# Kernel tuning notes

Measured on AMD Instinct MI355X. Metric: run time of the kernel, lower is better.

Reference implementation:

```python
import jax, jax.numpy as jnp
import numpy as np

EPS = 1e-12  # matches torch F.normalize eps default scale behavior (1e-12)

def _l2_normalize(x):
    n = jnp.sqrt(jnp.sum(x * x, axis=-1, keepdims=True))
    return x / jnp.maximum(n, EPS)

def setup_inputs() -> dict:
    key = jax.random.key(0)
    k1, k2 = jax.random.split(key)
    B, K, D = 32768, 4096, 1024
    context_repr = jax.random.normal(k1, (B, D), dtype=jnp.float32)
    # matches nn.init.normal_(std=0.02)
    cluster_centers = 0.02 * jax.random.normal(k2, (K, D), dtype=jnp.float32)
    return {"context_repr": context_repr, "cluster_centers": cluster_centers}

def reference(context_repr, cluster_centers):
    # L2-normalize rows of both
    x = _l2_normalize(context_repr)        # [B, D]
    c = _l2_normalize(cluster_centers)     # [K, D]
    x2 = jnp.sum(x * x, axis=-1, keepdims=True)          # [B, 1]
    c2 = jnp.sum(c * c, axis=-1)[None, :]                # [1, K]
    d2 = x2 + c2 - 2.0 * jnp.einsum('bd,kd->bk', x, c)   # [B, K]
    hard = jnp.argmin(d2, axis=-1)                       # [B]
    # Gather the UN-normalized learnable centers (as in the torch code)
    cluster_embedding = cluster_centers[hard]            # [B, D]
    return cluster_embedding
```

## Files before the change

### kernel.cpp

```cpp
#include <hip/hip_runtime.h>
#include <stdint.h>

#define B_ROWS 32768
#define K_CENT 4096
#define D_DIM  1024
#define EPS_CAND 5e-4f

typedef unsigned short u16;
typedef __attribute__((ext_vector_type(8))) __bf16 bf16x8;
typedef __attribute__((ext_vector_type(4))) float f32x4;

__device__ inline u16 f32_to_bf16(float f) {
    unsigned u = __float_as_uint(f);
    u += 0x7FFFu + ((u >> 16) & 1u);
    return (u16)(u >> 16);
}
__device__ inline float bf16_to_f32(u16 h) {
    return __uint_as_float(((unsigned)h) << 16);
}
__device__ inline unsigned ord_of_f32(float f) {
    unsigned u = __float_as_uint(f);
    return (u & 0x80000000u) ? ~u : (u | 0x80000000u);
}
__device__ inline float f32_of_ord(unsigned o) {
    unsigned u = (o & 0x80000000u) ? (o & 0x7fffffffu) : ~o;
    return __uint_as_float(u);
}

__global__ __launch_bounds__(256) void prep_rows(
    const float* __restrict__ src, u16* __restrict__ hi, u16* __restrict__ lo,
    float* __restrict__ sq, float* __restrict__ den)
{
    __shared__ double sm[4];
    const int row = blockIdx.x, tid = threadIdx.x;
    const float4 v = reinterpret_cast<const float4*>(src + (size_t)row * D_DIM)[tid];
    double ss = (double)v.x * v.x + (double)v.y * v.y
              + (double)v.z * v.z + (double)v.w * v.w;
#pragma unroll
    for (int m = 1; m < 64; m <<= 1) ss += __shfl_xor(ss, m, 64);
    if ((tid & 63) == 0) sm[tid >> 6] = ss;
    __syncthreads();
    const double tot = sm[0] + sm[1] + sm[2] + sm[3];
    const float d = fmaxf(sqrtf((float)tot), 1e-12f);
    const float n0 = v.x / d, n1 = v.y / d, n2 = v.z / d, n3 = v.w / d;

    ushort4 h, l;
    h.x = f32_to_bf16(n0); l.x = f32_to_bf16(n0 - bf16_to_f32(h.x));
    h.y = f32_to_bf16(n1); l.y = f32_to_bf16(n1 - bf16_to_f32(h.y));
    h.z = f32_to_bf16(n2); l.z = f32_to_bf16(n2 - bf16_to_f32(h.z));
    h.w = f32_to_bf16(n3); l.w = f32_to_bf16(n3 - bf16_to_f32(h.w));
    reinterpret_cast<ushort4*>(hi + (size_t)row * D_DIM)[tid] = h;
    reinterpret_cast<ushort4*>(lo + (size_t)row * D_DIM)[tid] = l;

    double s2 = (double)n0 * n0 + (double)n1 * n1
              + (double)n2 * n2 + (double)n3 * n3;
#pragma unroll
    for (int m = 1; m < 64; m <<= 1) s2 += __shfl_xor(s2, m, 64);
    __syncthreads();
    if ((tid & 63) == 0) sm[tid >> 6] = s2;
    __syncthreads();
    if (tid == 0) {
        sq[row] = (float)(sm[0] + sm[1] + sm[2] + sm[3]);
        den[row] = d;
    }
}

#define BM 128
#define BN 128
#define BK 32

__device__ inline void gload_lds16(const u16* g, u16* l) {
    __builtin_amdgcn_global_load_lds(
        (const __attribute__((address_space(1))) void*)g,
        (__attribute__((address_space(3))) void*)l, 16, 0, 0);
}

__global__ __launch_bounds__(256, 2) void gemm_cand(
    const u16* __restrict__ Ahi, const u16* __restrict__ Alo,
    const u16* __restrict__ Bhi, const u16* __restrict__ Blo,
    const float* __restrict__ c2, unsigned long long* __restrict__ cand)
{
    __shared__ u16 sAhi[BM * BK], sAlo[BM * BK];
    __shared__ u16 sBhi[BN * BK], sBlo[BN * BK];

    const int tid = threadIdx.x, lane = tid & 63, w = tid >> 6;

    const int flat = blockIdx.x;
    const int swz = (flat & 7) * 1024 + (flat >> 3);
    const int bx = swz & 31;
    const int by = swz >> 5;
    const size_t arow0 = (size_t)by * BM;
    const size_t brow0 = (size_t)bx * BN;

    const int p0 = w * 128 + lane, p1 = p0 + 64;
    const int r0 = p0 >> 2, cc0 = (p0 & 3) ^ ((r0 >> 1) & 3);
    const int r1 = p1 >> 2, cc1 = (p1 & 3) ^ ((r1 >> 1) & 3);
    const size_t aoff0 = (arow0 + r0) * D_DIM + cc0 * 8;
    const size_t aoff1 = (arow0 + r1) * D_DIM + cc1 * 8;
    const size_t boff0 = (brow0 + r0) * D_DIM + cc0 * 8;
    const size_t boff1 = (brow0 + r1) * D_DIM + cc1 * 8;
    const int ldst0 = w * 1024, ldst1 = ldst0 + 512;

    const int fr = lane & 15, fc = lane >> 4;
    int aoff_lds[4], boff_lds[4];
#pragma unroll
    for (int i = 0; i < 4; ++i) {
        const int ar = (w >> 1) * 64 + i * 16 + fr;
        aoff_lds[i] = ar * BK + ((fc ^ ((ar >> 1) & 3)) * 8);
        const int br = (w & 1) * 64 + i * 16 + fr;
        boff_lds[i] = br * BK + ((fc ^ ((br >> 1) & 3)) * 8);
    }

    f32x4 acc[4][4] = {};

    for (int kt = 0; kt < D_DIM / BK; ++kt) {
        const int k0 = kt * BK;
        __syncthreads();
        gload_lds16(Ahi + aoff0 + k0, sAhi + ldst0);
        gload_lds16(Ahi + aoff1 + k0, sAhi + ldst1);
        gload_lds16(Alo + aoff0 + k0, sAlo + ldst0);
        gload_lds16(Alo + aoff1 + k0, sAlo + ldst1);
        gload_lds16(Bhi + boff0 + k0, sBhi + ldst0);
        gload_lds16(Bhi + boff1 + k0, sBhi + ldst1);
        gload_lds16(Blo + boff0 + k0, sBlo + ldst0);
        gload_lds16(Blo + boff1 + k0, sBlo + ldst1);
        __syncthreads();

        bf16x8 ah[4], al[4], bh[4], bl[4];
#pragma unroll
        for (int i = 0; i < 4; ++i) {
            ah[i] = *reinterpret_cast<const bf16x8*>(sAhi + aoff_lds[i]);
            al[i] = *reinterpret_cast<const bf16x8*>(sAlo + aoff_lds[i]);
            bh[i] = *reinterpret_cast<const bf16x8*>(sBhi + boff_lds[i]);
            bl[i] = *reinterpret_cast<const bf16x8*>(sBlo + boff_lds[i]);
        }
#pragma unroll
        for (int mi = 0; mi < 4; ++mi)
#pragma unroll
            for (int ni = 0; ni < 4; ++ni)
                acc[mi][ni] = __builtin_amdgcn_mfma_f32_16x16x32_bf16(ah[mi], bh[ni], acc[mi][ni], 0, 0, 0);
#pragma unroll
        for (int mi = 0; mi < 4; ++mi)
#pragma unroll
            for (int ni = 0; ni < 4; ++ni)
                acc[mi][ni] = __builtin_amdgcn_mfma_f32_16x16x32_bf16(ah[mi], bl[ni], acc[mi][ni], 0, 0, 0);
#pragma unroll
        for (int mi = 0; mi < 4; ++mi)
#pragma unroll
            for (int ni = 0; ni < 4; ++ni)
                acc[mi][ni] = __builtin_amdgcn_mfma_f32_16x16x32_bf16(al[mi], bh[ni], acc[mi][ni], 0, 0, 0);
    }

    const int group = bx * 2 + (w & 1);
    float c2v[4];
#pragma unroll
    for (int ni = 0; ni < 4; ++ni)
        c2v[ni] = c2[brow0 + (w & 1) * 64 + ni * 16 + fr];

#pragma unroll
    for (int mi = 0; mi < 4; ++mi) {
#pragma unroll
        for (int r = 0; r < 4; ++r) {
            unsigned long long bk = ~0ull;
#pragma unroll
            for (int ni = 0; ni < 4; ++ni) {
                const float d2a = c2v[ni] - 2.0f * acc[mi][ni][r];
                const unsigned col = (unsigned)(brow0 + (w & 1) * 64 + ni * 16 + fr);
                const unsigned long long key =
                    ((unsigned long long)ord_of_f32(d2a) << 32) | col;
                if (key < bk) bk = key;
            }
#pragma unroll
            for (int ms = 1; ms < 16; ms <<= 1) {
                const unsigned long long o = __shfl_xor(bk, ms, 64);
                if (o < bk) bk = o;
            }
            if (fr == 0) {
                const size_t grow = arow0 + (w >> 1) * 64 + mi * 16 + fc * 4 + r;
                cand[grow * 64 + group] = bk;
            }
        }
    }
}

__global__ __launch_bounds__(256) void finalize(
    const unsigned long long* __restrict__ cand,
    const float* __restrict__ X, const float* __restrict__ C,
    const float* __restrict__ denx, const float* __restrict__ denc,
    const float* __restrict__ x2, const float* __restrict__ c2,
    float* __restrict__ out)
{
    const int w = threadIdx.x >> 6, lane = threadIdx.x & 63;
    const size_t row = (size_t)blockIdx.x * 4 + w;

    const unsigned long long v = cand[row * 64 + lane];
    unsigned long long m = v;
#pragma unroll
    for (int ms = 1; ms < 64; ms <<= 1) {
        const unsigned long long o = __shfl_xor(m, ms, 64);
        if (o < m) m = o;
    }
    const float fmin = f32_of_ord((unsigned)(m >> 32));
    const bool is_cand = f32_of_ord((unsigned)(v >> 32)) <= fmin + EPS_CAND;
    const unsigned long long ball = __ballot(is_cand);

    unsigned win;
    if (__popcll(ball) == 1) {
        win = (unsigned)(m & 0xffffffffu);
    } else {
        const float dxr = denx[row];
        const float x2r = x2[row];
        float xv[16];
#pragma unroll
        for (int j = 0; j < 16; ++j)
            xv[j] = X[row * D_DIM + j * 64 + lane] / dxr;

        float bestd2 = __uint_as_float(0x7f800000u);
        unsigned bwin = 0xffffffffu;
        unsigned long long bb = ball;
        while (bb) {
            const int l = __ffsll((unsigned long long)bb) - 1;
            bb &= bb - 1;
            const unsigned col = (unsigned)(__shfl(v, l, 64) & 0xffffffffu);
            const float dcr = denc[col];
            double s = 0.0;
#pragma unroll
            for (int j = 0; j < 16; ++j) {
                const float cv = C[(size_t)col * D_DIM + j * 64 + lane] / dcr;
                s = fma((double)xv[j], (double)cv, s);
            }
#pragma unroll
            for (int ms = 1; ms < 64; ms <<= 1) s += __shfl_xor(s, ms, 64);
            const float dotf = (float)s;
            const float d2 = (x2r + c2[col]) - 2.0f * dotf;
            if (d2 < bestd2 || (d2 == bestd2 && col < bwin)) {
                bestd2 = d2; bwin = col;
            }
        }
        win = bwin;
    }

    const float4* s4 = reinterpret_cast<const float4*>(C + (size_t)win * D_DIM);
    float4* d4 = reinterpret_cast<float4*>(out + row * D_DIM);
#pragma unroll
    for (int t = 0; t < 4; ++t) d4[t * 64 + lane] = s4[t * 64 + lane];
}

extern "C" void kernel_launch(void* const* d_in, const int* in_sizes, int n_in,
                              void* d_out, int out_size, void* d_ws, size_t ws_size,
                              hipStream_t stream)
{
    (void)in_sizes; (void)n_in; (void)out_size; (void)ws_size;
    const float* X = (const float*)d_in[0];
    const float* C = (const float*)d_in[1];
    float* out = (float*)d_out;

    char* ws = (char*)d_ws;
    u16* Ahi = (u16*)ws;
    u16* Alo = Ahi + (size_t)B_ROWS * D_DIM;
    u16* Bhi = Alo + (size_t)B_ROWS * D_DIM;
    u16* Blo = Bhi + (size_t)K_CENT * D_DIM;
    unsigned long long* cand =
        (unsigned long long*)(Blo + (size_t)K_CENT * D_DIM);
    float* c2   = (float*)(cand + (size_t)B_ROWS * 64);
    float* x2   = c2 + K_CENT;
    float* denx = x2 + B_ROWS;
    float* denc = denx + B_ROWS;

    prep_rows<<<B_ROWS, 256, 0, stream>>>(X, Ahi, Alo, x2, denx);
    prep_rows<<<K_CENT, 256, 0, stream>>>(C, Bhi, Blo, c2, denc);
    gemm_cand<<<(B_ROWS / BM) * (K_CENT / BN), 256, 0, stream>>>(
        Ahi, Alo, Bhi, Blo, c2, cand);
    finalize<<<B_ROWS / 4, 256, 0, stream>>>(
        cand, X, C, denx, denc, x2, c2, out);
}
```

Before: 1.022 ms.

## Triple-buffer GEMM LDS with 512-thread 256x128 tiles and split-phase prefetch

Rewrites the split-bf16 candidate GEMM to use 256x128 block tiles with 8 waves and a three-stage LDS ring buffer. Global-to-LDS loads for tile t+2 are issued between two half-phases of MFMA work, with explicit vmcnt waits, s_barrier and setprio, so memory traffic overlaps compute instead of waiting on a full barrier every k-step. The grid swizzle also snakes the column order on odd rows to improve L2 reuse. It uses more LDS (about 144KB for two blocks per CU) and relies on hand-placed waitcnt counts being exactly right.

```diff
diff --git a/kernel.cpp b/kernel.cpp
--- a/kernel.cpp
+++ b/kernel.cpp
@@ -65,97 +65,147 @@
     }
 }
 
-#define BM 128
+#define BM 256
 #define BN 128
 #define BK 32
-
-__device__ inline void gload_lds16(const u16* g, u16* l) {
-    __builtin_amdgcn_global_load_lds(
-        (const __attribute__((address_space(1))) void*)g,
-        (__attribute__((address_space(3))) void*)l, 16, 0, 0);
-}
-
-__global__ __launch_bounds__(256, 2) void gemm_cand(
+#define NT (D_DIM / BK)
+#define REG_U16 4096
+#define TILE_U16 (6 * REG_U16)
+
+__global__ __launch_bounds__(512, 2) void gemm_cand(
     const u16* __restrict__ Ahi, const u16* __restrict__ Alo,
     const u16* __restrict__ Bhi, const u16* __restrict__ Blo,
     const float* __restrict__ c2, unsigned long long* __restrict__ cand)
 {
-    __shared__ u16 sAhi[BM * BK], sAlo[BM * BK];
-    __shared__ u16 sBhi[BN * BK], sBlo[BN * BK];
+    __shared__ u16 lds[3 * TILE_U16];
 
     const int tid = threadIdx.x, lane = tid & 63, w = tid >> 6;
+    const int wm = w >> 1, wn = w & 1;
+    const int fr = lane & 15, fc = lane >> 4;
 
     const int flat = blockIdx.x;
-    const int swz = (flat & 7) * 1024 + (flat >> 3);
-    const int bx = swz & 31;
+    const int swz = (flat & 7) * 512 + (flat >> 3);
+    int bx = swz & 31;
     const int by = swz >> 5;
+    if (by & 1) bx = 31 - bx;
     const size_t arow0 = (size_t)by * BM;
     const size_t brow0 = (size_t)bx * BN;
 
-    const int p0 = w * 128 + lane, p1 = p0 + 64;
-    const int r0 = p0 >> 2, cc0 = (p0 & 3) ^ ((r0 >> 1) & 3);
-    const int r1 = p1 >> 2, cc1 = (p1 & 3) ^ ((r1 >> 1) & 3);
-    const size_t aoff0 = (arow0 + r0) * D_DIM + cc0 * 8;
-    const size_t aoff1 = (arow0 + r1) * D_DIM + cc1 * 8;
-    const size_t boff0 = (brow0 + r0) * D_DIM + cc0 * 8;
-    const size_t boff1 = (brow0 + r1) * D_DIM + cc1 * 8;
-    const int ldst0 = w * 1024, ldst1 = ldst0 + 512;
-
-    const int fr = lane & 15, fc = lane >> 4;
-    int aoff_lds[4], boff_lds[4];
+    const int p = w * 64 + lane;
+    const int srow = p >> 2;
+    const int scc = (p & 3) ^ ((srow >> 1) & 3);
+    const u16* gsrc[6];
+    gsrc[0] = Ahi + (arow0 + srow) * D_DIM + scc * 8;
+    gsrc[1] = Ahi + (arow0 + 128 + srow) * D_DIM + scc * 8;
+    gsrc[2] = Alo + (arow0 + srow) * D_DIM + scc * 8;
+    gsrc[3] = Alo + (arow0 + 128 + srow) * D_DIM + scc * 8;
+    gsrc[4] = Bhi + (brow0 + srow) * D_DIM + scc * 8;
+    gsrc[5] = Blo + (brow0 + srow) * D_DIM + scc * 8;
+    const int ldw = w * 512;
+
+    int offA[4], offB[4];
 #pragma unroll
     for (int i = 0; i < 4; ++i) {
-        const int ar = (w >> 1) * 64 + i * 16 + fr;
-        aoff_lds[i] = ar * BK + ((fc ^ ((ar >> 1) & 3)) * 8);
-        const int br = (w & 1) * 64 + i * 16 + fr;
-        boff_lds[i] = br * BK + ((fc ^ ((br >> 1) & 3)) * 8);
+        const int ar = wm * 64 + i * 16 + fr;
+        const int rg = ar >> 7, rr = ar & 127;
+        offA[i] = rg * REG_U16 + rr * 32 + ((fc ^ ((rr >> 1) & 3)) * 8);
+        const int br = wn * 64 + i * 16 + fr;
+        offB[i] = br * 32 + ((fc ^ ((br >> 1) & 3)) * 8);
     }
 
     f32x4 acc[4][4] = {};
 
-    for (int kt = 0; kt < D_DIM / BK; ++kt) {
-        const int k0 = kt * BK;
-        __syncthreads();
-        gload_lds16(Ahi + aoff0 + k0, sAhi + ldst0);
-        gload_lds16(Ahi + aoff1 + k0, sAhi + ldst1);
-        gload_lds16(Alo + aoff0 + k0, sAlo + ldst0);
-        gload_lds16(Alo + aoff1 + k0, sAlo + ldst1);
-        gload_lds16(Bhi + boff0 + k0, sBhi + ldst0);
-        gload_lds16(Bhi + boff1 + k0, sBhi + ldst1);
-        gload_lds16(Blo + boff0 + k0, sBlo + ldst0);
-        gload_lds16(Blo + boff1 + k0, sBlo + ldst1);
-        __syncthreads();
-
-        bf16x8 ah[4], al[4], bh[4], bl[4];
-#pragma unroll
-        for (int i = 0; i < 4; ++i) {
-            ah[i] = *reinterpret_cast<const bf16x8*>(sAhi + aoff_lds[i]);
-            al[i] = *reinterpret_cast<const bf16x8*>(sAlo + aoff_lds[i]);
-            bh[i] = *reinterpret_cast<const bf16x8*>(sBhi + boff_lds[i]);
-            bl[i] = *reinterpret_cast<const bf16x8*>(sBlo + boff_lds[i]);
-        }
-#pragma unroll
-        for (int mi = 0; mi < 4; ++mi)
-#pragma unroll
-            for (int ni = 0; ni < 4; ++ni)
-                acc[mi][ni] = __builtin_amdgcn_mfma_f32_16x16x32_bf16(ah[mi], bh[ni], acc[mi][ni], 0, 0, 0);
-#pragma unroll
-        for (int mi = 0; mi < 4; ++mi)
-#pragma unroll
-            for (int ni = 0; ni < 4; ++ni)
-                acc[mi][ni] = __builtin_amdgcn_mfma_f32_16x16x32_bf16(ah[mi], bl[ni], acc[mi][ni], 0, 0, 0);
-#pragma unroll
-        for (int mi = 0; mi < 4; ++mi)
-#pragma unroll
-            for (int ni = 0; ni < 4; ++ni)
-                acc[mi][ni] = __builtin_amdgcn_mfma_f32_16x16x32_bf16(al[mi], bh[ni], acc[mi][ni], 0, 0, 0);
-    }
-
-    const int group = bx * 2 + (w & 1);
+#define STAGE3(t, J0)                                                         \
+    do {                                                                      \
+        const int _base = ((t) % 3) * TILE_U16;                               \
+        const int _k = (t) * BK;                                              \
+        _Pragma("unroll")                                                     \
+        for (int _j = (J0); _j < (J0) + 3; ++_j)                              \
+            __builtin_amdgcn_global_load_lds(                                 \
+                (const __attribute__((address_space(1))) void*)(gsrc[_j] + _k), \
+                (__attribute__((address_space(3))) void*)(lds + _base + _j * REG_U16 + ldw), \
+                16, 0, 0);                                                    \
+    } while (0)
+
+    STAGE3(0, 0); STAGE3(0, 3);
+    STAGE3(1, 0); STAGE3(1, 3);
+    asm volatile("s_waitcnt vmcnt(6)" ::: "memory");
+    __builtin_amdgcn_s_barrier();
+
+    for (int t = 0; t < NT; ++t) {
+        const int cb = (t % 3) * TILE_U16;
+
+        bf16x8 bhf[4], blf[4], ah0[2], al0[2];
+#pragma unroll
+        for (int n = 0; n < 4; ++n) {
+            bhf[n] = *reinterpret_cast<const bf16x8*>(lds + cb + 4 * REG_U16 + offB[n]);
+            blf[n] = *reinterpret_cast<const bf16x8*>(lds + cb + 5 * REG_U16 + offB[n]);
+        }
+#pragma unroll
+        for (int i = 0; i < 2; ++i) {
+            ah0[i] = *reinterpret_cast<const bf16x8*>(lds + cb + offA[i]);
+            al0[i] = *reinterpret_cast<const bf16x8*>(lds + cb + 2 * REG_U16 + offA[i]);
+        }
+        if (t + 2 < NT) STAGE3(t + 2, 0);
+        __builtin_amdgcn_sched_barrier(0);
+        __builtin_amdgcn_s_barrier();
+        __builtin_amdgcn_s_setprio(1);
+#pragma unroll
+        for (int i = 0; i < 2; ++i)
+#pragma unroll
+            for (int n = 0; n < 4; ++n)
+                acc[i][n] = __builtin_amdgcn_mfma_f32_16x16x32_bf16(ah0[i], bhf[n], acc[i][n], 0, 0, 0);
+#pragma unroll
+        for (int i = 0; i < 2; ++i)
+#pragma unroll
+            for (int n = 0; n < 4; ++n)
+                acc[i][n] = __builtin_amdgcn_mfma_f32_16x16x32_bf16(ah0[i], blf[n], acc[i][n], 0, 0, 0);
+#pragma unroll
+        for (int i = 0; i < 2; ++i)
+#pragma unroll
+            for (int n = 0; n < 4; ++n)
+                acc[i][n] = __builtin_amdgcn_mfma_f32_16x16x32_bf16(al0[i], bhf[n], acc[i][n], 0, 0, 0);
+        __builtin_amdgcn_s_setprio(0);
+        __builtin_amdgcn_s_barrier();
+
+        bf16x8 ah1[2], al1[2];
+#pragma unroll
+        for (int i = 0; i < 2; ++i) {
+            ah1[i] = *reinterpret_cast<const bf16x8*>(lds + cb + offA[2 + i]);
+            al1[i] = *reinterpret_cast<const bf16x8*>(lds + cb + 2 * REG_U16 + offA[2 + i]);
+        }
+        if (t + 2 < NT) STAGE3(t + 2, 3);
+        __builtin_amdgcn_sched_barrier(0);
+        __builtin_amdgcn_s_barrier();
+        __builtin_amdgcn_s_setprio(1);
+#pragma unroll
+        for (int i = 0; i < 2; ++i)
+#pragma unroll
+            for (int n = 0; n < 4; ++n)
+                acc[2 + i][n] = __builtin_amdgcn_mfma_f32_16x16x32_bf16(ah1[i], bhf[n], acc[2 + i][n], 0, 0, 0);
+#pragma unroll
+        for (int i = 0; i < 2; ++i)
+#pragma unroll
+            for (int n = 0; n < 4; ++n)
+                acc[2 + i][n] = __builtin_amdgcn_mfma_f32_16x16x32_bf16(ah1[i], blf[n], acc[2 + i][n], 0, 0, 0);
+#pragma unroll
+        for (int i = 0; i < 2; ++i)
+#pragma unroll
+            for (int n = 0; n < 4; ++n)
+                acc[2 + i][n] = __builtin_amdgcn_mfma_f32_16x16x32_bf16(al1[i], bhf[n], acc[2 + i][n], 0, 0, 0);
+        __builtin_amdgcn_s_setprio(0);
+
+        if (t < NT - 2)       asm volatile("s_waitcnt vmcnt(6)" ::: "memory");
+        else if (t == NT - 2) asm volatile("s_waitcnt vmcnt(0)" ::: "memory");
+        if (t < NT - 1) __builtin_amdgcn_s_barrier();
+    }
+#undef STAGE3
+
+    const int group = bx * 2 + wn;
     float c2v[4];
 #pragma unroll
-    for (int ni = 0; ni < 4; ++ni)
-        c2v[ni] = c2[brow0 + (w & 1) * 64 + ni * 16 + fr];
+    for (int n = 0; n < 4; ++n)
+        c2v[n] = c2[brow0 + wn * 64 + n * 16 + fr];
 
 #pragma unroll
     for (int mi = 0; mi < 4; ++mi) {
@@ -165,7 +215,7 @@
 #pragma unroll
             for (int ni = 0; ni < 4; ++ni) {
                 const float d2a = c2v[ni] - 2.0f * acc[mi][ni][r];
-                const unsigned col = (unsigned)(brow0 + (w & 1) * 64 + ni * 16 + fr);
+                const unsigned col = (unsigned)(brow0 + wn * 64 + ni * 16 + fr);
                 const unsigned long long key =
                     ((unsigned long long)ord_of_f32(d2a) << 32) | col;
                 if (key < bk) bk = key;
@@ -176,7 +226,7 @@
                 if (o < bk) bk = o;
             }
             if (fr == 0) {
-                const size_t grow = arow0 + (w >> 1) * 64 + mi * 16 + fc * 4 + r;
+                const size_t grow = arow0 + wm * 64 + mi * 16 + fc * 4 + r;
                 cand[grow * 64 + group] = bk;
             }
         }
@@ -269,7 +319,7 @@
 
     prep_rows<<<B_ROWS, 256, 0, stream>>>(X, Ahi, Alo, x2, denx);
     prep_rows<<<K_CENT, 256, 0, stream>>>(C, Bhi, Blo, c2, denc);
-    gemm_cand<<<(B_ROWS / BM) * (K_CENT / BN), 256, 0, stream>>>(
+    gemm_cand<<<(B_ROWS / BM) * (K_CENT / BN), 512, 0, stream>>>(
         Ahi, Alo, Bhi, Blo, c2, cand);
     finalize<<<B_ROWS / 4, 256, 0, stream>>>(
         cand, X, C, denx, denc, x2, c2, out);
```

After: 1.060 ms. 1.04x slower.
